# Kernel tuning notes

Measured on AMD Instinct MI355X. Metric: run time of the kernel, lower is better.

The kernel has to match this reference:

```python
import jax, jax.numpy as jnp
import numpy as np

STU, ITEM, CONC, D = 50000, 20000, 2000, 128
E_CC, E_IC, E_SI = 40000, 80000, 1000000


def _gat(tgt_x, src_x, e_src, e_dst, n_tgt, W, att_l, att_r, slope=0.2):
    # single-head GATConv, aggr='add', concat with heads=1 -> [n_tgt, D]
    if W is not None:
        xl = src_x @ W.T  # lin_l applied to source
        xr = tgt_x @ W.T  # lin_l shared for target (in_channels is int)
        # noqa: torch module uses lin_l for both when in_channels is int
    else:
        xl, xr = src_x, tgt_x
    sl = xl @ att_l  # [n_src]
    sr = xr @ att_r  # [n_tgt]
    e = sl[e_src] + sr[e_dst]
    e = jnp.where(e > 0, e, slope * e)  # leaky_relu
    # segment softmax over edges grouped by target node
    m = jax.ops.segment_max(e, e_dst, num_segments=n_tgt)
    m = jnp.where(jnp.isfinite(m), m, 0.0)
    ex = jnp.exp(e - m[e_dst])
    den = jax.ops.segment_sum(ex, e_dst, num_segments=n_tgt) + 1e-16
    alpha = ex / den[e_dst]
    return jax.ops.segment_sum(xl[e_src] * alpha[:, None], e_dst, num_segments=n_tgt)


def setup_inputs():
    key = jax.random.key(0)
    ks = jax.random.split(key, 40)
    s = 1.0 / np.sqrt(D)
    n = lambda k, sh, sc=1.0: jax.random.normal(k, sh, jnp.float32) * sc
    return {
        'stu_x': n(ks[0], (STU, D)),
        'item_x': n(ks[1], (ITEM, D)),
        'conc_x': n(ks[2], (CONC, D)),
        'stu_raw_x': n(ks[3], (STU, D)),
        'W_cc': n(ks[4], (D, D), s), 'al_cc': n(ks[5], (D,), s), 'ar_cc': n(ks[6], (D,), s),
        'W_ic': n(ks[7], (D, D), s), 'al_ic': n(ks[8], (D,), s), 'ar_ic': n(ks[9], (D,), s),
        'al_cce': n(ks[10], (D,), s), 'ar_cce': n(ks[11], (D,), s),
        'al_ice': n(ks[12], (D,), s), 'ar_ice': n(ks[13], (D,), s),
        'W_ci': n(ks[14], (D, D), s), 'al_ci': n(ks[15], (D,), s), 'ar_ci': n(ks[16], (D,), s),
        'W_si': n(ks[17], (D, D), s), 'al_si': n(ks[18], (D,), s), 'ar_si': n(ks[19], (D,), s),
        'w_ci_att': n(ks[20], (2 * D,), s), 'w_si_att': n(ks[21], (2 * D,), s),
        'W_is': n(ks[22], (D, D), s), 'al_is': n(ks[23], (D,), s), 'ar_is': n(ks[24], (D,), s),
        'cc_src': jax.random.randint(ks[25], (E_CC,), 0, CONC),
        'cc_dst': jax.random.randint(ks[26], (E_CC,), 0, CONC),
        'ic_item': jax.random.randint(ks[27], (E_IC,), 0, ITEM),
        'ic_conc': jax.random.randint(ks[28], (E_IC,), 0, CONC),
        'si_stu': jax.random.randint(ks[29], (E_SI,), 0, STU),
        'si_item': jax.random.randint(ks[30], (E_SI,), 0, ITEM),
    }


def reference(stu_x, item_x, conc_x, stu_raw_x,
              W_cc, al_cc, ar_cc, W_ic, al_ic, ar_ic,
              al_cce, ar_cce, al_ice, ar_ice,
              W_ci, al_ci, ar_ci, W_si, al_si, ar_si,
              w_ci_att, w_si_att, W_is, al_is, ar_is,
              cc_src, cc_dst, ic_item, ic_conc, si_stu, si_item):
    # --- concept fusion ---
    c1 = _gat(conc_x, conc_x, cc_src, cc_dst, CONC, W_cc, al_cc, ar_cc)   # inter_conc_conc
    c2 = _gat(conc_x, item_x, ic_item, ic_conc, CONC, W_ic, al_ic, ar_ic) # inter_item_conc
    e1 = _gat(conc_x, c1, cc_src, cc_dst, CONC, None, al_cce, ar_cce)     # exter_conc_conc (no lin)
    e2 = _gat(conc_x, c2, cc_src, cc_dst, CONC, None, al_ice, ar_ice)     # exter_item_conc (no lin)
    conc_fused = conc_x + e1 + e2
    # --- item fusion ---
    i1 = _gat(item_x, conc_x, ic_conc, ic_item, ITEM, W_ci, al_ci, ar_ci) # inter_conc_item
    i2 = _gat(item_x, stu_x, si_stu, si_item, ITEM, W_si, al_si, ar_si)   # inter_stu_item
    # softmax over dim=1 of an [N,1] tensor (as in the torch code): equals 1.0
    att1 = jax.nn.softmax((jnp.concatenate([i1, item_x], axis=1) @ w_ci_att)[:, None], axis=1)
    att2 = jax.nn.softmax((jnp.concatenate([i2, item_x], axis=1) @ w_si_att)[:, None], axis=1)
    item_fused = item_x + att1 * i1 + att2 * i2
    # --- student fusion (uses raw data['stu'].x as target) ---
    s1 = _gat(stu_raw_x, item_x, si_item, si_stu, STU, W_is, al_is, ar_is)
    stu_fused = stu_raw_x + s1
    return (conc_fused, item_fused, stu_fused)
```

## Files before the change

kernel.cpp:

```cpp
#include <hip/hip_runtime.h>

#define CONC_N 2000
#define ITEM_N 20000
#define STU_N  50000
#define NE_CC  40000
#define NE_IC  80000
#define NE_SI  1000000
#define TBUCK  382

typedef unsigned int uint;
typedef unsigned short ushort;
typedef signed char s8;
typedef __attribute__((ext_vector_type(8))) short bf16x8;
typedef __attribute__((ext_vector_type(4))) float f32x4;

__device__ __forceinline__ ushort f2bf(float f) {
  uint u = __float_as_uint(f);
  uint r = (u + 0x7FFFu + ((u >> 16) & 1u)) >> 16;
  return (ushort)r;
}

__device__ __forceinline__ bf16x8 packfrag(float4 lo, float4 hi) {
  union { bf16x8 s; uint u[4]; } p;
  p.u[0] = (uint)f2bf(lo.x) | ((uint)f2bf(lo.y) << 16);
  p.u[1] = (uint)f2bf(lo.z) | ((uint)f2bf(lo.w) << 16);
  p.u[2] = (uint)f2bf(hi.x) | ((uint)f2bf(hi.y) << 16);
  p.u[3] = (uint)f2bf(hi.z) | ((uint)f2bf(hi.w) << 16);
  return p.s;
}


struct CsrG {
  const int* dst; const int* src;
  unsigned* keys; int* srcs; int* offs;
  int E, n, shift, nbuck, tb, sb;
};
struct CsrGs { CsrG g[5]; };


struct ProjDesc { const float* W; const float* a; float* out; };
struct SetupArgs {
  ProjDesc p[10];
  CsrGs G;
  int* pcnt;
  const float* wsrc[5];
  ushort* wdst[5];
};

__global__ __launch_bounds__(256) void setup_k(SetupArgs A) {
  int b = blockIdx.x;
  int tid = threadIdx.x;
  if (b < 10) {
    __shared__ float Wl[128 * 132];
    __shared__ float a_s[128];
    ProjDesc d = A.p[b];
    #pragma unroll
    for (int i = 0; i < 16; ++i) {
      int s = tid + i * 256;
      int row = s >> 5, c4 = s & 31;
      float4 w = *(const float4*)&d.W[s * 4];
      float* dst = &Wl[row * 132 + c4 * 4];
      dst[0] = w.x; dst[1] = w.y; dst[2] = w.z; dst[3] = w.w;
    }
    if (tid < 128) a_s[tid] = d.a[tid];
    __syncthreads();
    if (tid < 128) {
      float acc = 0.f;
      #pragma unroll 4
      for (int j = 0; j < 128; ++j) acc += Wl[j * 132 + tid] * a_s[j];
      d.out[tid] = acc;
    }
    return;
  }
  if (b >= 170) {
    int wi = b - 170;
    const float* Ws = A.wsrc[wi];
    ushort* Wd = A.wdst[wi];
    for (int rec = tid; rec < 2048; rec += 256) {
      int lane = rec & 63;
      int kk = (rec >> 6) & 3;
      int nt = rec >> 8;
      int x = lane & 15, g = lane >> 4;
      const float* src = &Ws[(nt * 16 + x) * 128 + kk * 32 + 4 * g];
      float4 lo = *(const float4*)src;
      float4 hi = *(const float4*)(src + 16);
      bf16x8 pk = packfrag(lo, hi);
      *(bf16x8*)&Wd[rec * 8] = pk;
    }
    return;
  }
  int bsel = b - 10;
  int gi = bsel >> 5, blk = bsel & 31;
  CsrG g = A.G.g[gi];
  __shared__ int lcnt[128];
  if (tid < 128) lcnt[tid] = 0;
  __syncthreads();
  int chunk = (g.E + 31) >> 5;
  int e0 = blk * chunk, e1 = min(g.E, e0 + chunk);
  for (int e = e0 + tid; e < e1; e += 256)
    atomicAdd(&lcnt[g.dst[e] >> g.shift], 1);
  __syncthreads();
  if (tid < 128) A.pcnt[bsel * 128 + tid] = lcnt[tid];
}


__global__ __launch_bounds__(512) void csr_scan(CsrGs G, const int* __restrict__ pcnt,
                                                int* __restrict__ cur, int* __restrict__ bases) {
  __shared__ int lc[TBUCK];
  __shared__ int lb[TBUCK + 5];
  int tid = threadIdx.x, lane = tid & 63, wv = tid >> 6;
  if (tid < TBUCK) {
    int gi = 0;
    #pragma unroll
    for (int k = 1; k < 5; ++k) if (tid >= G.g[k].tb) gi = k;
    int b = tid - G.g[gi].tb;
    int s = 0;
    for (int blk = 0; blk < 32; ++blk) s += pcnt[((gi << 5) + blk) * 128 + b];
    lc[tid] = s;
  }
  __syncthreads();
  if (wv < 5) {
    CsrG g = G.g[wv];
    int carry = 0;
    for (int base = 0; base < g.nbuck; base += 64) {
      int idx = base + lane;
      int v = (idx < g.nbuck) ? lc[g.tb + idx] : 0;
      int incl = v;
      #pragma unroll
      for (int o = 1; o < 64; o <<= 1) {
        int y = __shfl_up(incl, o);
        if (lane >= o) incl += y;
      }
      if (idx < g.nbuck) lb[g.sb + idx] = carry + incl - v;
      carry += __shfl(incl, 63);
    }
    if (lane == 0) lb[g.sb + g.nbuck] = carry;
  }
  __syncthreads();
  if (tid < TBUCK + 5) bases[tid] = lb[tid];
  if (tid < TBUCK) {
    int gi = 0;
    for (int k = 1; k < 5; ++k) if (tid >= G.g[k].tb) gi = k;
    cur[tid] = lb[tid + gi];
  }
  if (tid < 5) G.g[tid].offs[G.g[tid].n] = G.g[tid].E;
}


__device__ void partition_body(const CsrGs& G, int* __restrict__ cur, int gi, int bx,
                               int nbx, unsigned char* smem) {
  CsrG g = G.g[gi];
  unsigned* ck = (unsigned*)smem;
  unsigned char* cb = smem + 16384;
  int* lcnt = (int*)(smem + 20480);
  int* lcur = (int*)(smem + 20992);
  int tid = threadIdx.x;
  unsigned dmask = (1u << g.shift) - 1;
  for (int c0 = bx * 4096; c0 < g.E; c0 += nbx * 4096) {
    if (tid < 128) lcnt[tid] = 0;
    __syncthreads();
    #pragma unroll
    for (int i = 0; i < 16; ++i) {
      int e = c0 + i * 256 + tid;
      if (e < g.E) {
        int d = g.dst[e], s = g.src[e];
        int b = d >> g.shift;
        ck[i * 256 + tid] = ((unsigned)(d & dmask) << 16) | (unsigned)s;
        cb[i * 256 + tid] = (unsigned char)b;
        atomicAdd(&lcnt[b], 1);
      } else cb[i * 256 + tid] = 255;
    }
    __syncthreads();
    if (tid < g.nbuck && lcnt[tid] > 0) lcur[tid] = atomicAdd(&cur[g.tb + tid], lcnt[tid]);
    __syncthreads();
    #pragma unroll
    for (int i = 0; i < 16; ++i) {
      int b = cb[i * 256 + tid];
      if (b != 255) {
        int pos = atomicAdd(&lcur[b], 1);
        g.keys[pos] = ck[i * 256 + tid];
      }
    }
    __syncthreads();
  }
}

__device__ void rdot_body(const float* __restrict__ x, const float* __restrict__ v,
                          float* __restrict__ o, int n, int blk, int nblk) {
  int lane = threadIdx.x & 63;
  int wid = (blk * 256 + threadIdx.x) >> 6;
  int nw = nblk * 4;
  float va = v[lane], vb = v[64 + lane];
  for (int r = wid; r < n; r += nw) {
    float a = x[r * 128 + lane] * va + x[r * 128 + 64 + lane] * vb;
    #pragma unroll
    for (int of = 32; of; of >>= 1) a += __shfl_xor(a, of);
    if (lane == 0) o[r] = a;
  }
}

__global__ __launch_bounds__(256) void mid3_k(CsrGs G, int* cur,
                                              const float* rx, const float* rv,
                                              float* ro, int rnb) {
  __shared__ __align__(16) unsigned char smem[21504];
  int b = blockIdx.x;
  if (b < 600) {
    partition_body(G, cur, b / 120, b % 120, 120, smem);
  } else {
    rdot_body(rx, rv, ro, STU_N, b - 600, rnb);
  }
}


struct GemmDesc { const float* X; s8* Y8; float2* SS; int n, b0;
                  const float* dv[6]; float* dq[6]; int ds[6]; };
struct BigC {
  GemmDesc g[5];
  int gemm_blocks;
};

__device__ void build_lite(const CsrGs& G, const int* __restrict__ bases, int bid,
                           int* lh, int* lex, int* lcu, int* wsum) {
  int gi = 0;
  for (int k = 1; k < 5; ++k) if (bid >= G.g[k].tb) gi = k;
  CsrG g = G.g[gi];
  int b = bid - g.tb;
  int base = bases[g.sb + b];
  int cnt = bases[g.sb + b + 1] - base;

  int tid = threadIdx.x;
  lh[tid] = 0; lh[tid + 256] = 0;
  __syncthreads();
  for (int j = tid; j < cnt; j += 256)
    atomicAdd(&lh[g.keys[base + j] >> 16], 1);
  __syncthreads();
  int a0 = lh[2 * tid], a1 = lh[2 * tid + 1];
  int pair = a0 + a1;
  int lane = tid & 63, wv = tid >> 6;
  int incl = pair;
  #pragma unroll
  for (int o = 1; o < 64; o <<= 1) {
    int y = __shfl_up(incl, o);
    if (lane >= o) incl += y;
  }
  if (lane == 63) wsum[wv] = incl;
  __syncthreads();
  if (tid == 0) {
    int s = 0;
    #pragma unroll
    for (int w = 0; w < 4; ++w) { int t = wsum[w]; wsum[w] = s; s += t; }
  }
  __syncthreads();
  int ep = wsum[wv] + incl - pair;
  lex[2 * tid] = ep;       lex[2 * tid + 1] = ep + a0;
  lcu[2 * tid] = ep;       lcu[2 * tid + 1] = ep + a0;
  __syncthreads();
  int dst0 = b << g.shift;
  int ndst = min(1 << g.shift, g.n - dst0);
  for (int dl = tid; dl < ndst; dl += 256) g.offs[dst0 + dl] = base + lex[dl];
  for (int j = tid; j < cnt; j += 256) {
    unsigned k = g.keys[base + j];
    int dl = k >> 16;
    int pos = atomicAdd(&lcu[dl], 1);
    g.srcs[base + pos] = (int)(k & 0xFFFFu);
  }
}

template <int NV>
__device__ void gemm_bodyT(const GemmDesc& gd, const ushort* __restrict__ Wf, int blk) {
  int tid = threadIdx.x;
  int lane = tid & 63, wv = tid >> 6;
  int x = lane & 15, g = lane >> 4;
  int row = blk * 64 + wv * 16 + x;
  const float* xr = &gd.X[(size_t)(row < gd.n ? row : 0) * 128];
  bf16x8 afrag[4];
  float dacc[NV == 0 ? 1 : NV];
  #pragma unroll
  for (int v = 0; v < NV; ++v) dacc[v] = 0.f;
  #pragma unroll
  for (int kk = 0; kk < 4; ++kk) {
    float4 lo = *(const float4*)&xr[kk * 32 + 4 * g];
    float4 hi = *(const float4*)&xr[kk * 32 + 16 + 4 * g];
    afrag[kk] = packfrag(lo, hi);
    #pragma unroll
    for (int v = 0; v < NV; ++v) {
      const float* vp = gd.dv[v];
      float4 vlo = *(const float4*)&vp[kk * 32 + 4 * g];
      float4 vhi = *(const float4*)&vp[kk * 32 + 16 + 4 * g];
      dacc[v] += lo.x * vlo.x + lo.y * vlo.y + lo.z * vlo.z + lo.w * vlo.w
               + hi.x * vhi.x + hi.y * vhi.y + hi.z * vhi.z + hi.w * vhi.w;
    }
  }
  #pragma unroll
  for (int v = 0; v < NV; ++v) {
    float dsum = dacc[v];
    dsum += __shfl_xor(dsum, 16);
    dsum += __shfl_xor(dsum, 32);
    if (lane < 16 && row < gd.n) gd.dq[v][(size_t)row * gd.ds[v]] = dsum;
  }
  f32x4 acc[8];
  #pragma unroll
  for (int t = 0; t < 8; ++t) acc[t] = (f32x4){0.f, 0.f, 0.f, 0.f};
  #pragma unroll
  for (int nt = 0; nt < 8; ++nt) {
    #pragma unroll
    for (int kk = 0; kk < 4; ++kk) {
      union { uint4 u; bf16x8 s; } bu;
      bu.u = *(const uint4*)&Wf[(size_t)((nt * 4 + kk) * 64 + lane) * 8];
      acc[nt] = __builtin_amdgcn_mfma_f32_16x16x32_bf16(afrag[kk], bu.s, acc[nt], 0, 0, 0);
    }
  }
  int orow = blk * 64 + wv * 16 + 4 * g;
  #pragma unroll
  for (int r = 0; r < 4; ++r) {
    float m8 = 0.f;
    #pragma unroll
    for (int nt = 0; nt < 8; ++nt) m8 = fmaxf(m8, fabsf(acc[nt][r]));
    #pragma unroll
    for (int msk = 1; msk < 16; msk <<= 1) m8 = fmaxf(m8, __shfl_xor(m8, msk));
    int gr = orow + r;
    if (gr < gd.n) {
      float invs = (m8 > 0.f) ? 127.f / m8 : 0.f;
      if (x == 0) gd.SS[gr].y = m8 * (1.f / 127.f);
      #pragma unroll
      for (int nt = 0; nt < 8; ++nt) {
        int q = (int)rintf(acc[nt][r] * invs);
        gd.Y8[(size_t)gr * 128 + nt * 16 + x] = (s8)q;
      }
    }
  }
}

__global__ __launch_bounds__(256, 2) void mid4_k(CsrGs G, const int* bases, BigC C,
                                                 const ushort* W0, const ushort* W1,
                                                 const ushort* W2, const ushort* W3,
                                                 const ushort* W4) {
  __shared__ int lh[512], lex[512], lcu[512], wsum[4];
  int b = blockIdx.x;
  if (b < TBUCK) {
    build_lite(G, bases, b, lh, lex, lcu, wsum);
    return;
  }
  b -= TBUCK;
  if (b < C.g[1].b0)      gemm_bodyT<6>(C.g[0], W0, b - C.g[0].b0);
  else if (b < C.g[2].b0) gemm_bodyT<4>(C.g[1], W1, b - C.g[1].b0);
  else if (b < C.g[3].b0) gemm_bodyT<0>(C.g[2], W2, b - C.g[2].b0);
  else if (b < C.g[4].b0) gemm_bodyT<1>(C.g[3], W3, b - C.g[3].b0);
  else                    gemm_bodyT<0>(C.g[4], W4, b - C.g[4].b0);
}


__device__ __forceinline__ void fma8q(float acc[8], float wj, uint2 u) {
  int lo = (int)u.x, hi = (int)u.y;
  acc[0] += wj * (float)((lo << 24) >> 24);
  acc[1] += wj * (float)((lo << 16) >> 24);
  acc[2] += wj * (float)((lo << 8) >> 24);
  acc[3] += wj * (float)(lo >> 24);
  acc[4] += wj * (float)((hi << 24) >> 24);
  acc[5] += wj * (float)((hi << 16) >> 24);
  acc[6] += wj * (float)((hi << 8) >> 24);
  acc[7] += wj * (float)(hi >> 24);
}

__device__ void gat_core16(const int* __restrict__ offs, const int* __restrict__ srcs,
                           const float2* __restrict__ ssc, const float* __restrict__ sr,
                           const s8* __restrict__ x8,
                           int t4, int n_tgt, int lane, float acc[8]) {
  int q = lane >> 4, il = lane & 15;
  int t = t4 + q;
  bool tv = t < n_tgt;
  int sbeg = tv ? offs[t] : 0;
  int send = tv ? offs[t + 1] : 0;
  float srt = tv ? sr[t] : 0.f;

  float se = 0.f;
  #pragma unroll
  for (int r = 0; r < 8; ++r) acc[r] = 0.f;
  int qb = q << 4;

  for (int i0 = sbeg; i0 < send; i0 += 16) {
    int cnt = min(16, send - i0);
// ... 111 lines not shown
  #pragma unroll
  for (int o = 32; o; o >>= 1) {
    se1 += __shfl_xor(se1, o);
    se2 += __shfl_xor(se2, o);
  }
  float inv1 = 1.f / (se1 + 1e-16f), inv2 = 1.f / (se2 + 1e-16f);
  float ax = 0.f, ay = 0.f;
  for (int i0 = sbeg; i0 < send; i0 += 64) {
    int cnt = min(64, send - i0);
    int s = 0; float w1 = 0.f, w2 = 0.f;
    if (lane < cnt) {
      s = srcs[i0 + lane];
      float e1 = sl1[s] + srt1; e1 = e1 > 0.f ? e1 : 0.2f * e1;
      float e2 = sl2[s] + srt2; e2 = e2 > 0.f ? e2 : 0.2f * e2;
      w1 = __expf(e1 - m1) * inv1;
      w2 = __expf(e2 - m2) * inv2;
    }
    for (int j = 0; j < cnt; ++j) {
      int sj = __shfl(s, j);
      float wj1 = __shfl(w1, j);
      float wj2 = __shfl(w2, j);
      const float2 v1 = *(const float2*)&xl1[sj * 128 + lane * 2];
      const float2 v2 = *(const float2*)&xl2[sj * 128 + lane * 2];
      ax += wj1 * v1.x + wj2 * v2.x;
      ay += wj1 * v1.y + wj2 * v2.y;
    }
  }
  const float2 b = *(const float2*)&base[t * 128 + lane * 2];
  float2 o2; o2.x = ax + b.x; o2.y = ay + b.y;
  *(float2*)&out[t * 128 + lane * 2] = o2;
}


#define NB_I12 1250
#define NB_S1  3125
#define NB_CC  125

struct GatsArgs {
  const int *offs4, *srcs4; const float2* ssc_is; const float* sr_is;
  const s8* x_is; const float* stu_raw_x; float* out_stu;
  const int *offs3, *srcs3; const float2* ssc_si; const float* sr_si; const s8* x_si;
  const int *offs2, *srcs2; const float2* ssc_ci; const float* sr_ci; const s8* x_ci;
  const float* item_x; float* out_item;
  const int *offs0, *srcs0; const float2* ssc_cc; const float* sr_cc; const s8* x_cc;
  const float* al_cce; float *c1, *sl_cce;
  const int *offs1, *srcs1; const float2* ssc_ic; const float* sr_ic; const s8* x_ic;
  const float* al_ice; float *c2, *sl_ice;
};

__global__ void gats_k(GatsArgs A) {
  int b = blockIdx.x;
  int lane = threadIdx.x & 63;
  int wv = threadIdx.x >> 6;
  if (b < NB_I12) {
    int t4 = b * 16 + wv * 4;
    float acc1[8], acc2[8];
    gat_core16(A.offs2, A.srcs2, A.ssc_ci, A.sr_ci, A.x_ci, t4, ITEM_N, lane, acc1);
    gat_core16(A.offs3, A.srcs3, A.ssc_si, A.sr_si, A.x_si, t4, ITEM_N, lane, acc2);
    #pragma unroll
    for (int r = 0; r < 8; ++r) acc1[r] += acc2[r];
    gat_store16(acc1, A.item_x, A.out_item, t4, ITEM_N, lane);
  } else if (b < NB_I12 + NB_S1) {
    int t4 = (b - NB_I12) * 16 + wv * 4;
    float acc[8];
    gat_core16(A.offs4, A.srcs4, A.ssc_is, A.sr_is, A.x_is, t4, STU_N, lane, acc);
    gat_store16(acc, A.stu_raw_x, A.out_stu, t4, STU_N, lane);
  } else {
    int sub = b - NB_I12 - NB_S1;
    int which = sub >= NB_CC;
    int t4 = (sub - which * NB_CC) * 16 + wv * 4;
    if (!which)
      c1c2_body16(A.offs0, A.srcs0, A.ssc_cc, A.sr_cc, A.x_cc, A.al_cce,
                  A.c1, A.sl_cce, t4, CONC_N, lane);
    else
      c1c2_body16(A.offs1, A.srcs1, A.ssc_ic, A.sr_ic, A.x_ic, A.al_ice,
                  A.c2, A.sl_ice, t4, CONC_N, lane);
  }
}


__global__ void fin_k(const int* offs0, const int* srcs0,
                      const float* sl_cce, const float* sr_cce, const float* c1,
                      const float* sl_ice, const float* sr_ice, const float* c2,
                      const float* conc_x, float* out_conc) {
  int t = (blockIdx.x * blockDim.x + threadIdx.x) >> 6;
  if (t >= CONC_N) return;
  gat_dual_core(offs0, srcs0, sl_cce, sr_cce, c1, sl_ice, sr_ice, c2,
                conc_x, out_conc, t, threadIdx.x & 63);
}


extern "C" void kernel_launch(void* const* d_in, const int* in_sizes, int n_in,
                              void* d_out, int out_size, void* d_ws, size_t ws_size,
                              hipStream_t stream) {
  const float* stu_x     = (const float*)d_in[0];
  const float* item_x    = (const float*)d_in[1];
  const float* conc_x    = (const float*)d_in[2];
  const float* stu_raw_x = (const float*)d_in[3];
  const float* W_cc  = (const float*)d_in[4];
  const float* al_cc = (const float*)d_in[5];
  const float* ar_cc = (const float*)d_in[6];
  const float* W_ic  = (const float*)d_in[7];
  const float* al_ic = (const float*)d_in[8];
  const float* ar_ic = (const float*)d_in[9];
  const float* al_cce = (const float*)d_in[10];
  const float* ar_cce = (const float*)d_in[11];
  const float* al_ice = (const float*)d_in[12];
  const float* ar_ice = (const float*)d_in[13];
  const float* W_ci  = (const float*)d_in[14];
  const float* al_ci = (const float*)d_in[15];
  const float* ar_ci = (const float*)d_in[16];
  const float* W_si  = (const float*)d_in[17];
  const float* al_si = (const float*)d_in[18];
  const float* ar_si = (const float*)d_in[19];
  const float* W_is  = (const float*)d_in[22];
  const float* al_is = (const float*)d_in[23];
  const float* ar_is = (const float*)d_in[24];
  const int* cc_src  = (const int*)d_in[25];
  const int* cc_dst  = (const int*)d_in[26];
  const int* ic_item = (const int*)d_in[27];
  const int* ic_conc = (const int*)d_in[28];
// ... 27 lines not shown
  float* sr_ic  = (float*)alloc(CONC_N * 4);
  float* sr_ci  = (float*)alloc(ITEM_N * 4);
  float* sr_si  = (float*)alloc(ITEM_N * 4);
  float* sr_is  = (float*)alloc(STU_N * 4);
  float* sl_cce = (float*)alloc(CONC_N * 4);
  float* sr_cce = (float*)alloc(CONC_N * 4);
  float* sl_ice = (float*)alloc(CONC_N * 4);
  float* sr_ice = (float*)alloc(CONC_N * 4);

  unsigned* keys0 = (unsigned*)alloc((size_t)NE_CC * 4);
  unsigned* keys1 = (unsigned*)alloc((size_t)NE_IC * 4);
  unsigned* keys2 = (unsigned*)alloc((size_t)NE_IC * 4);
  unsigned* keys3 = (unsigned*)alloc((size_t)NE_SI * 4);
  unsigned* keys4 = (unsigned*)alloc((size_t)NE_SI * 4);
  int* srcs0 = (int*)alloc((size_t)NE_CC * 4);
  int* srcs1 = (int*)alloc((size_t)NE_IC * 4);
  int* srcs2 = (int*)alloc((size_t)NE_IC * 4);
  int* srcs3 = (int*)alloc((size_t)NE_SI * 4);
  int* srcs4 = (int*)alloc((size_t)NE_SI * 4);
  int* offs0 = (int*)alloc((CONC_N + 1) * 4);
  int* offs1 = (int*)alloc((CONC_N + 1) * 4);
  int* offs2 = (int*)alloc((ITEM_N + 1) * 4);
  int* offs3 = (int*)alloc((ITEM_N + 1) * 4);
  int* offs4 = (int*)alloc((STU_N + 1) * 4);
  int* pcnt      = (int*)alloc(5 * 32 * 128 * 4);
  int* cur_all   = (int*)alloc(TBUCK * 4);
  int* bases_all = (int*)alloc((TBUCK + 5) * 4);

  float* out = (float*)d_out;
  float* out_conc = out;
  float* out_item = out + (size_t)CONC_N * 128;
  float* out_stu  = out + (size_t)(CONC_N + ITEM_N) * 128;

  CsrGs G;
  G.g[0] = {cc_dst,  cc_src,  keys0, srcs0, offs0, NE_CC, CONC_N, 5, 63,   0,   0};
  G.g[1] = {ic_conc, ic_item, keys1, srcs1, offs1, NE_IC, CONC_N, 5, 63,  63,  64};
  G.g[2] = {ic_item, ic_conc, keys2, srcs2, offs2, NE_IC, ITEM_N, 8, 79, 126, 128};
  G.g[3] = {si_item, si_stu,  keys3, srcs3, offs3, NE_SI, ITEM_N, 8, 79, 205, 208};
  G.g[4] = {si_stu,  si_item, keys4, srcs4, offs4, NE_SI, STU_N,  9, 98, 284, 288};

  SetupArgs SA;
  SA.p[0] = {W_cc, al_cc, vecs + 0 * 128};
  SA.p[1] = {W_cc, ar_cc, vecs + 1 * 128};
  SA.p[2] = {W_ic, al_ic, vecs + 2 * 128};
  SA.p[3] = {W_ic, ar_ic, vecs + 3 * 128};
  SA.p[4] = {W_ci, al_ci, vecs + 4 * 128};
  SA.p[5] = {W_ci, ar_ci, vecs + 5 * 128};
  SA.p[6] = {W_si, al_si, vecs + 6 * 128};
  SA.p[7] = {W_si, ar_si, vecs + 7 * 128};
  SA.p[8] = {W_is, al_is, vecs + 8 * 128};
  SA.p[9] = {W_is, ar_is, vecs + 9 * 128};
  SA.G = G;
  SA.pcnt = pcnt;
  SA.wsrc[0] = W_cc; SA.wsrc[1] = W_ic; SA.wsrc[2] = W_ci;
  SA.wsrc[3] = W_si; SA.wsrc[4] = W_is;
  for (int i = 0; i < 5; ++i) SA.wdst[i] = Wbf[i];
  setup_k<<<175, 256, 0, stream>>>(SA);

  csr_scan<<<1, 512, 0, stream>>>(G, pcnt, cur_all, bases_all);

  mid3_k<<<600 + 1024, 256, 0, stream>>>(G, cur_all, stu_raw_x, vecs + 9 * 128,
                                         sr_is, 1024);

  BigC C;
  C.g[0] = {conc_x, concWcc, ssc_cc, CONC_N, 0,
            {vecs + 0 * 128, vecs + 1 * 128, vecs + 3 * 128, vecs + 4 * 128, ar_cce, ar_ice},
            {(float*)ssc_cc, sr_cc, sr_ic, (float*)ssc_ci, sr_cce, sr_ice},
            {2, 1, 1, 2, 1, 1}};
  C.g[1] = {item_x, itemWic, ssc_ic, ITEM_N, 32,
            {vecs + 2 * 128, vecs + 5 * 128, vecs + 7 * 128, vecs + 8 * 128, nullptr, nullptr},
            {(float*)ssc_ic, sr_ci, sr_si, (float*)ssc_is, nullptr, nullptr},
            {2, 1, 1, 2, 1, 1}};
  C.g[2] = {conc_x, concWci, ssc_ci, CONC_N, 345,
            {nullptr, nullptr, nullptr, nullptr, nullptr, nullptr},
            {nullptr, nullptr, nullptr, nullptr, nullptr, nullptr},
            {1, 1, 1, 1, 1, 1}};
  C.g[3] = {stu_x, stuWsi, ssc_si, STU_N, 377,
            {vecs + 6 * 128, nullptr, nullptr, nullptr, nullptr, nullptr},
            {(float*)ssc_si, nullptr, nullptr, nullptr, nullptr, nullptr},
            {2, 1, 1, 1, 1, 1}};
  C.g[4] = {item_x, itemWis, ssc_is, ITEM_N, 1159,
            {nullptr, nullptr, nullptr, nullptr, nullptr, nullptr},
            {nullptr, nullptr, nullptr, nullptr, nullptr, nullptr},
            {1, 1, 1, 1, 1, 1}};
  C.gemm_blocks = 1472;
  mid4_k<<<TBUCK + 1472, 256, 0, stream>>>(G, bases_all, C,
                                           Wbf[0], Wbf[1], Wbf[2], Wbf[3], Wbf[4]);

  GatsArgs GA;
  GA.offs4 = offs4; GA.srcs4 = srcs4; GA.ssc_is = ssc_is; GA.sr_is = sr_is;
  GA.x_is = itemWis; GA.stu_raw_x = stu_raw_x; GA.out_stu = out_stu;
  GA.offs3 = offs3; GA.srcs3 = srcs3; GA.ssc_si = ssc_si; GA.sr_si = sr_si;
  GA.x_si = stuWsi;
  GA.offs2 = offs2; GA.srcs2 = srcs2; GA.ssc_ci = ssc_ci; GA.sr_ci = sr_ci;
  GA.x_ci = concWci; GA.item_x = item_x; GA.out_item = out_item;
  GA.offs0 = offs0; GA.srcs0 = srcs0; GA.ssc_cc = ssc_cc; GA.sr_cc = sr_cc;
  GA.x_cc = concWcc; GA.al_cce = al_cce; GA.c1 = c1buf; GA.sl_cce = sl_cce;
  GA.offs1 = offs1; GA.srcs1 = srcs1; GA.ssc_ic = ssc_ic; GA.sr_ic = sr_ic;
  GA.x_ic = itemWic; GA.al_ice = al_ice; GA.c2 = c2buf; GA.sl_ice = sl_ice;
  gats_k<<<NB_I12 + NB_S1 + 2 * NB_CC, 256, 0, stream>>>(GA);

  fin_k<<<500, 256, 0, stream>>>(offs0, srcs0, sl_cce, sr_cce, c1buf,
                                 sl_ice, sr_ice, c2buf, conc_x, out_conc);
}
```

Baseline: 173.9 us.

## Fuse all stages into one cooperative persistent kernel with grid syncs

Replaces the six separate kernel launches with a single cooperative kernel that loops over virtual block ids per phase and separates phases with grid.sync(). The build_lite stage is moved out of the GEMM kernel into its own phase after partitioning, and the small projection now reads W directly from global memory instead of staging it in LDS. The goal is to remove launch gaps and per-kernel tail effects. In exchange, the grid size is capped by occupancy, grid-wide barriers add their own cost, the single-block scan phase idles the rest of the grid, and the separate-kernel path is kept as a fallback.

```diff
diff --git a/kernel.cpp b/kernel.cpp
--- a/kernel.cpp
+++ b/kernel.cpp
@@ -1,4 +1,7 @@
 #include <hip/hip_runtime.h>
+#include <hip/hip_cooperative_groups.h>
+
+namespace cg = cooperative_groups;
 
 #define CONC_N 2000
 #define ITEM_N 20000
@@ -8,6 +11,16 @@
 #define NE_SI  1000000
 #define TBUCK  382
 
+#define NB_PART 600
+#define NB_GEMM 1472
+#define NB_RDOT 1024
+#define NB_B    (NB_PART + NB_GEMM + NB_RDOT)
+#define NB_I12  1250
+#define NB_S1   3125
+#define NB_CC   125
+#define NB_D    (NB_I12 + NB_S1 + 2 * NB_CC)
+#define NB_E    500
+
 typedef unsigned int uint;
 typedef unsigned short ushort;
 typedef signed char s8;
@@ -37,62 +50,70 @@
 };
 struct CsrGs { CsrG g[5]; };
 
-
 struct ProjDesc { const float* W; const float* a; float* out; };
-struct SetupArgs {
+
+struct GemmDesc { const float* X; s8* Y8; float2* SS; int n, b0;
+                  const float* dv[6]; float* dq[6]; int ds[6]; };
+struct BigC { GemmDesc g[5]; };
+
+struct GatsArgs {
+  const int *offs4, *srcs4; const float2* ssc_is; const float* sr_is;
+  const s8* x_is; const float* stu_raw_x; float* out_stu;
+  const int *offs3, *srcs3; const float2* ssc_si; const float* sr_si; const s8* x_si;
+  const int *offs2, *srcs2; const float2* ssc_ci; const float* sr_ci; const s8* x_ci;
+  const float* item_x; float* out_item;
+  const int *offs0, *srcs0; const float2* ssc_cc; const float* sr_cc; const s8* x_cc;
+  const float* al_cce; float *c1, *sl_cce;
+  const int *offs1, *srcs1; const float2* ssc_ic; const float* sr_ic; const s8* x_ic;
+  const float* al_ice; float *c2, *sl_ice;
+};
+
+struct MegaArgs {
   ProjDesc p[10];
   CsrGs G;
   int* pcnt;
   const float* wsrc[5];
   ushort* wdst[5];
+  int* cur; int* bases;
+  BigC C;
+  const float* rx; const float* rv; float* ro;
+  GatsArgs GA;
+  const float* sr_cce; const float* sr_ice;
+  const float* conc_x; float* out_conc;
 };
 
-__global__ __launch_bounds__(256) void setup_k(SetupArgs A) {
-  int b = blockIdx.x;
+
+__device__ void proj_body(const ProjDesc& d) {
   int tid = threadIdx.x;
-  if (b < 10) {
-    __shared__ float Wl[128 * 132];
-    __shared__ float a_s[128];
-    ProjDesc d = A.p[b];
-    #pragma unroll
-    for (int i = 0; i < 16; ++i) {
-      int s = tid + i * 256;
-      int row = s >> 5, c4 = s & 31;
-      float4 w = *(const float4*)&d.W[s * 4];
-      float* dst = &Wl[row * 132 + c4 * 4];
-      dst[0] = w.x; dst[1] = w.y; dst[2] = w.z; dst[3] = w.w;
-    }
-    if (tid < 128) a_s[tid] = d.a[tid];
-    __syncthreads();
-    if (tid < 128) {
-      float acc = 0.f;
-      #pragma unroll 4
-      for (int j = 0; j < 128; ++j) acc += Wl[j * 132 + tid] * a_s[j];
-      d.out[tid] = acc;
-    }
-    return;
-  }
-  if (b >= 170) {
-    int wi = b - 170;
-    const float* Ws = A.wsrc[wi];
-    ushort* Wd = A.wdst[wi];
-    for (int rec = tid; rec < 2048; rec += 256) {
-      int lane = rec & 63;
-      int kk = (rec >> 6) & 3;
-      int nt = rec >> 8;
-      int x = lane & 15, g = lane >> 4;
-      const float* src = &Ws[(nt * 16 + x) * 128 + kk * 32 + 4 * g];
-      float4 lo = *(const float4*)src;
-      float4 hi = *(const float4*)(src + 16);
-      bf16x8 pk = packfrag(lo, hi);
-      *(bf16x8*)&Wd[rec * 8] = pk;
-    }
-    return;
-  }
-  int bsel = b - 10;
+  if (tid < 128) {
+    float acc = 0.f;
+    #pragma unroll 4
+    for (int j = 0; j < 128; ++j) acc += d.W[j * 128 + tid] * d.a[j];
+    d.out[tid] = acc;
+  }
+}
+
+__device__ void wconv_body(const float* __restrict__ Ws, ushort* __restrict__ Wd) {
+  int tid = threadIdx.x;
+  for (int rec = tid; rec < 2048; rec += 256) {
+    int lane = rec & 63;
+    int kk = (rec >> 6) & 3;
+    int nt = rec >> 8;
+    int x = lane & 15, g = lane >> 4;
+    const float* src = &Ws[(nt * 16 + x) * 128 + kk * 32 + 4 * g];
+    float4 lo = *(const float4*)src;
+    float4 hi = *(const float4*)(src + 16);
+    bf16x8 pk = packfrag(lo, hi);
+    *(bf16x8*)&Wd[rec * 8] = pk;
+  }
+}
+
+__device__ void hist_body(const CsrGs& G, int* __restrict__ pcnt, int bsel,
+                          unsigned char* smem) {
+  int* lcnt = (int*)smem;
+  int tid = threadIdx.x;
   int gi = bsel >> 5, blk = bsel & 31;
-  CsrG g = A.G.g[gi];
-  __shared__ int lcnt[128];
+  CsrG g = G.g[gi];
   if (tid < 128) lcnt[tid] = 0;
   __syncthreads();
   int chunk = (g.E + 31) >> 5;
@@ -100,52 +121,56 @@
   for (int e = e0 + tid; e < e1; e += 256)
     atomicAdd(&lcnt[g.dst[e] >> g.shift], 1);
   __syncthreads();
-  if (tid < 128) A.pcnt[bsel * 128 + tid] = lcnt[tid];
-}
-
-
-__global__ __launch_bounds__(512) void csr_scan(CsrGs G, const int* __restrict__ pcnt,
-                                                int* __restrict__ cur, int* __restrict__ bases) {
-  __shared__ int lc[TBUCK];
-  __shared__ int lb[TBUCK + 5];
-  int tid = threadIdx.x, lane = tid & 63, wv = tid >> 6;
-  if (tid < TBUCK) {
+  if (tid < 128) pcnt[bsel * 128 + tid] = lcnt[tid];
+  __syncthreads();
+}
+
+__device__ void scan_body(const CsrGs& G, const int* __restrict__ pcnt,
+                          int* __restrict__ cur, int* __restrict__ bases,
+                          unsigned char* smem) {
+  int* lc = (int*)smem;
+  int* lb = (int*)(smem + 2048);
+  int tid = threadIdx.x;
+  for (int i = tid; i < TBUCK; i += 256) {
     int gi = 0;
     #pragma unroll
-    for (int k = 1; k < 5; ++k) if (tid >= G.g[k].tb) gi = k;
-    int b = tid - G.g[gi].tb;
+    for (int k = 1; k < 5; ++k) if (i >= G.g[k].tb) gi = k;
+    int b = i - G.g[gi].tb;
     int s = 0;
     for (int blk = 0; blk < 32; ++blk) s += pcnt[((gi << 5) + blk) * 128 + b];
-    lc[tid] = s;
-  }
-  __syncthreads();
-  if (wv < 5) {
-    CsrG g = G.g[wv];
-    int carry = 0;
-    for (int base = 0; base < g.nbuck; base += 64) {
-      int idx = base + lane;
-      int v = (idx < g.nbuck) ? lc[g.tb + idx] : 0;
-      int incl = v;
-      #pragma unroll
-      for (int o = 1; o < 64; o <<= 1) {
-        int y = __shfl_up(incl, o);
-        if (lane >= o) incl += y;
+    lc[i] = s;
+  }
+  __syncthreads();
+  int lane = tid & 63, wv = tid >> 6;
+  if (wv == 0) {
+    for (int gi = 0; gi < 5; ++gi) {
+      CsrG g = G.g[gi];
+      int carry = 0;
+      for (int base = 0; base < g.nbuck; base += 64) {
+        int idx = base + lane;
+        int v = (idx < g.nbuck) ? lc[g.tb + idx] : 0;
+        int incl = v;
+        #pragma unroll
+        for (int o = 1; o < 64; o <<= 1) {
+          int y = __shfl_up(incl, o);
+          if (lane >= o) incl += y;
+        }
+        if (idx < g.nbuck) lb[g.sb + idx] = carry + incl - v;
+        carry += __shfl(incl, 63);
       }
-      if (idx < g.nbuck) lb[g.sb + idx] = carry + incl - v;
-      carry += __shfl(incl, 63);
-    }
-    if (lane == 0) lb[g.sb + g.nbuck] = carry;
-  }
-  __syncthreads();
-  if (tid < TBUCK + 5) bases[tid] = lb[tid];
-  if (tid < TBUCK) {
+      if (lane == 0) lb[g.sb + g.nbuck] = carry;
+    }
+  }
+  __syncthreads();
+  for (int i = tid; i < TBUCK + 5; i += 256) bases[i] = lb[i];
+  for (int i = tid; i < TBUCK; i += 256) {
     int gi = 0;
-    for (int k = 1; k < 5; ++k) if (tid >= G.g[k].tb) gi = k;
-    cur[tid] = lb[tid + gi];
+    for (int k = 1; k < 5; ++k) if (i >= G.g[k].tb) gi = k;
+    cur[i] = lb[i + gi];
   }
   if (tid < 5) G.g[tid].offs[G.g[tid].n] = G.g[tid].E;
-}
-
+  __syncthreads();
+}
 
 __device__ void partition_body(const CsrGs& G, int* __restrict__ cur, int gi, int bx,
                                int nbx, unsigned char* smem) {
@@ -199,73 +224,6 @@
   }
 }
 
-__global__ __launch_bounds__(256) void mid3_k(CsrGs G, int* cur,
-                                              const float* rx, const float* rv,
-                                              float* ro, int rnb) {
-  __shared__ __align__(16) unsigned char smem[21504];
-  int b = blockIdx.x;
-  if (b < 600) {
-    partition_body(G, cur, b / 120, b % 120, 120, smem);
-  } else {
-    rdot_body(rx, rv, ro, STU_N, b - 600, rnb);
-  }
-}
-
-
-struct GemmDesc { const float* X; s8* Y8; float2* SS; int n, b0;
-                  const float* dv[6]; float* dq[6]; int ds[6]; };
-struct BigC {
-  GemmDesc g[5];
-  int gemm_blocks;
-};
-
-__device__ void build_lite(const CsrGs& G, const int* __restrict__ bases, int bid,
-                           int* lh, int* lex, int* lcu, int* wsum) {
-  int gi = 0;
-  for (int k = 1; k < 5; ++k) if (bid >= G.g[k].tb) gi = k;
-  CsrG g = G.g[gi];
-  int b = bid - g.tb;
-  int base = bases[g.sb + b];
-  int cnt = bases[g.sb + b + 1] - base;
-
-  int tid = threadIdx.x;
-  lh[tid] = 0; lh[tid + 256] = 0;
-  __syncthreads();
-  for (int j = tid; j < cnt; j += 256)
-    atomicAdd(&lh[g.keys[base + j] >> 16], 1);
-  __syncthreads();
-  int a0 = lh[2 * tid], a1 = lh[2 * tid + 1];
-  int pair = a0 + a1;
-  int lane = tid & 63, wv = tid >> 6;
-  int incl = pair;
-  #pragma unroll
-  for (int o = 1; o < 64; o <<= 1) {
-    int y = __shfl_up(incl, o);
-    if (lane >= o) incl += y;
-  }
-  if (lane == 63) wsum[wv] = incl;
-  __syncthreads();
-  if (tid == 0) {
-    int s = 0;
-    #pragma unroll
-    for (int w = 0; w < 4; ++w) { int t = wsum[w]; wsum[w] = s; s += t; }
-  }
-  __syncthreads();
-  int ep = wsum[wv] + incl - pair;
-  lex[2 * tid] = ep;       lex[2 * tid + 1] = ep + a0;
-  lcu[2 * tid] = ep;       lcu[2 * tid + 1] = ep + a0;
-  __syncthreads();
-  int dst0 = b << g.shift;
-  int ndst = min(1 << g.shift, g.n - dst0);
-  for (int dl = tid; dl < ndst; dl += 256) g.offs[dst0 + dl] = base + lex[dl];
-  for (int j = tid; j < cnt; j += 256) {
-    unsigned k = g.keys[base + j];
-    int dl = k >> 16;
-    int pos = atomicAdd(&lcu[dl], 1);
-    g.srcs[base + pos] = (int)(k & 0xFFFFu);
-  }
-}
-
 template <int NV>
 __device__ void gemm_bodyT(const GemmDesc& gd, const ushort* __restrict__ Wf, int blk) {
   int tid = threadIdx.x;
@@ -331,22 +289,56 @@
   }
 }
 
-__global__ __launch_bounds__(256, 2) void mid4_k(CsrGs G, const int* bases, BigC C,
-                                                 const ushort* W0, const ushort* W1,
-                                                 const ushort* W2, const ushort* W3,
-                                                 const ushort* W4) {
-  __shared__ int lh[512], lex[512], lcu[512], wsum[4];
-  int b = blockIdx.x;
-  if (b < TBUCK) {
-    build_lite(G, bases, b, lh, lex, lcu, wsum);
-    return;
-  }
-  b -= TBUCK;
-  if (b < C.g[1].b0)      gemm_bodyT<6>(C.g[0], W0, b - C.g[0].b0);
-  else if (b < C.g[2].b0) gemm_bodyT<4>(C.g[1], W1, b - C.g[1].b0);
-  else if (b < C.g[3].b0) gemm_bodyT<0>(C.g[2], W2, b - C.g[2].b0);
-  else if (b < C.g[4].b0) gemm_bodyT<1>(C.g[3], W3, b - C.g[3].b0);
-  else                    gemm_bodyT<0>(C.g[4], W4, b - C.g[4].b0);
+__device__ void build_lite(const CsrGs& G, const int* __restrict__ bases, int bid,
+                           unsigned char* smem) {
+  int* lh = (int*)smem;
+  int* lex = (int*)(smem + 2048);
+  int* lcu = (int*)(smem + 4096);
+  int* wsum = (int*)(smem + 6144);
+  int gi = 0;
+  for (int k = 1; k < 5; ++k) if (bid >= G.g[k].tb) gi = k;
+  CsrG g = G.g[gi];
+  int b = bid - g.tb;
+  int base = bases[g.sb + b];
+  int cnt = bases[g.sb + b + 1] - base;
+
+  int tid = threadIdx.x;
+  lh[tid] = 0; lh[tid + 256] = 0;
+  __syncthreads();
+  for (int j = tid; j < cnt; j += 256)
+    atomicAdd(&lh[g.keys[base + j] >> 16], 1);
+  __syncthreads();
+  int a0 = lh[2 * tid], a1 = lh[2 * tid + 1];
+  int pair = a0 + a1;
+  int lane = tid & 63, wv = tid >> 6;
+  int incl = pair;
+  #pragma unroll
+  for (int o = 1; o < 64; o <<= 1) {
+    int y = __shfl_up(incl, o);
+    if (lane >= o) incl += y;
+  }
+  if (lane == 63) wsum[wv] = incl;
+  __syncthreads();
+  if (tid == 0) {
+    int s = 0;
+    #pragma unroll
+    for (int w = 0; w < 4; ++w) { int t = wsum[w]; wsum[w] = s; s += t; }
+  }
+  __syncthreads();
+  int ep = wsum[wv] + incl - pair;
+  lex[2 * tid] = ep;       lex[2 * tid + 1] = ep + a0;
+  lcu[2 * tid] = ep;       lcu[2 * tid + 1] = ep + a0;
+  __syncthreads();
+  int dst0 = b << g.shift;
+  int ndst = min(1 << g.shift, g.n - dst0);
+  for (int dl = tid; dl < ndst; dl += 256) g.offs[dst0 + dl] = base + lex[dl];
+  for (int j = tid; j < cnt; j += 256) {
+    unsigned k = g.keys[base + j];
+    int dl = k >> 16;
+    int pos = atomicAdd(&lcu[dl], 1);
+    g.srcs[base + pos] = (int)(k & 0xFFFFu);
+  }
+  __syncthreads();
 }
 
 
@@ -524,61 +516,106 @@
 }
 
 
-#define NB_I12 1250
-#define NB_S1  3125
-#define NB_CC  125
-
-struct GatsArgs {
-  const int *offs4, *srcs4; const float2* ssc_is; const float* sr_is;
-  const s8* x_is; const float* stu_raw_x; float* out_stu;
-  const int *offs3, *srcs3; const float2* ssc_si; const float* sr_si; const s8* x_si;
-  const int *offs2, *srcs2; const float2* ssc_ci; const float* sr_ci; const s8* x_ci;
-  const float* item_x; float* out_item;
-  const int *offs0, *srcs0; const float2* ssc_cc; const float* sr_cc; const s8* x_cc;
-  const float* al_cce; float *c1, *sl_cce;
-  const int *offs1, *srcs1; const float2* ssc_ic; const float* sr_ic; const s8* x_ic;
-  const float* al_ice; float *c2, *sl_ice;
-};
-
-__global__ void gats_k(GatsArgs A) {
-  int b = blockIdx.x;
+__device__ void phaseA(const MegaArgs& A, int vb, unsigned char* smem) {
+  if (vb < 10) proj_body(A.p[vb]);
+  else if (vb >= 170) wconv_body(A.wsrc[vb - 170], A.wdst[vb - 170]);
+  else hist_body(A.G, A.pcnt, vb - 10, smem);
+}
+
+__device__ void phaseB(const MegaArgs& A, int vb, unsigned char* smem) {
+  if (vb < NB_PART) {
+    partition_body(A.G, A.cur, vb / 120, vb % 120, 120, smem);
+  } else if (vb < NB_PART + NB_GEMM) {
+    int b = vb - NB_PART;
+    const BigC& C = A.C;
+    if (b < C.g[1].b0)      gemm_bodyT<6>(C.g[0], A.wdst[0], b - C.g[0].b0);
+    else if (b < C.g[2].b0) gemm_bodyT<4>(C.g[1], A.wdst[1], b - C.g[1].b0);
+    else if (b < C.g[3].b0) gemm_bodyT<0>(C.g[2], A.wdst[2], b - C.g[2].b0);
+    else if (b < C.g[4].b0) gemm_bodyT<1>(C.g[3], A.wdst[3], b - C.g[3].b0);
+    else                    gemm_bodyT<0>(C.g[4], A.wdst[4], b - C.g[4].b0);
+  } else {
+    rdot_body(A.rx, A.rv, A.ro, STU_N, vb - NB_PART - NB_GEMM, NB_RDOT);
+  }
+}
+
+__device__ void phaseD(const MegaArgs& A, int vb) {
+  const GatsArgs& GA = A.GA;
   int lane = threadIdx.x & 63;
   int wv = threadIdx.x >> 6;
-  if (b < NB_I12) {
-    int t4 = b * 16 + wv * 4;
+  if (vb < NB_I12) {
+    int t4 = vb * 16 + wv * 4;
     float acc1[8], acc2[8];
-    gat_core16(A.offs2, A.srcs2, A.ssc_ci, A.sr_ci, A.x_ci, t4, ITEM_N, lane, acc1);
-    gat_core16(A.offs3, A.srcs3, A.ssc_si, A.sr_si, A.x_si, t4, ITEM_N, lane, acc2);
+    gat_core16(GA.offs2, GA.srcs2, GA.ssc_ci, GA.sr_ci, GA.x_ci, t4, ITEM_N, lane, acc1);
+    gat_core16(GA.offs3, GA.srcs3, GA.ssc_si, GA.sr_si, GA.x_si, t4, ITEM_N, lane, acc2);
     #pragma unroll
     for (int r = 0; r < 8; ++r) acc1[r] += acc2[r];
-    gat_store16(acc1, A.item_x, A.out_item, t4, ITEM_N, lane);
-  } else if (b < NB_I12 + NB_S1) {
-    int t4 = (b - NB_I12) * 16 + wv * 4;
+    gat_store16(acc1, GA.item_x, GA.out_item, t4, ITEM_N, lane);
+  } else if (vb < NB_I12 + NB_S1) {
+    int t4 = (vb - NB_I12) * 16 + wv * 4;
     float acc[8];
-    gat_core16(A.offs4, A.srcs4, A.ssc_is, A.sr_is, A.x_is, t4, STU_N, lane, acc);
-    gat_store16(acc, A.stu_raw_x, A.out_stu, t4, STU_N, lane);
+    gat_core16(GA.offs4, GA.srcs4, GA.ssc_is, GA.sr_is, GA.x_is, t4, STU_N, lane, acc);
+    gat_store16(acc, GA.stu_raw_x, GA.out_stu, t4, STU_N, lane);
   } else {
-    int sub = b - NB_I12 - NB_S1;
+    int sub = vb - NB_I12 - NB_S1;
     int which = sub >= NB_CC;
     int t4 = (sub - which * NB_CC) * 16 + wv * 4;
     if (!which)
-      c1c2_body16(A.offs0, A.srcs0, A.ssc_cc, A.sr_cc, A.x_cc, A.al_cce,
-                  A.c1, A.sl_cce, t4, CONC_N, lane);
+      c1c2_body16(GA.offs0, GA.srcs0, GA.ssc_cc, GA.sr_cc, GA.x_cc, GA.al_cce,
+                  GA.c1, GA.sl_cce, t4, CONC_N, lane);
     else
-      c1c2_body16(A.offs1, A.srcs1, A.ssc_ic, A.sr_ic, A.x_ic, A.al_ice,
-                  A.c2, A.sl_ice, t4, CONC_N, lane);
-  }
-}
-
-
-__global__ void fin_k(const int* offs0, const int* srcs0,
-                      const float* sl_cce, const float* sr_cce, const float* c1,
-                      const float* sl_ice, const float* sr_ice, const float* c2,
-                      const float* conc_x, float* out_conc) {
-  int t = (blockIdx.x * blockDim.x + threadIdx.x) >> 6;
-  if (t >= CONC_N) return;
-  gat_dual_core(offs0, srcs0, sl_cce, sr_cce, c1, sl_ice, sr_ice, c2,
-                conc_x, out_conc, t, threadIdx.x & 63);
+      c1c2_body16(GA.offs1, GA.srcs1, GA.ssc_ic, GA.sr_ic, GA.x_ic, GA.al_ice,
+                  GA.c2, GA.sl_ice, t4, CONC_N, lane);
+  }
+}
+
+__device__ void phaseE(const MegaArgs& A, int vb) {
+  int t = (vb * 256 + (int)threadIdx.x) >> 6;
+  if (t < CONC_N)
+    gat_dual_core(A.GA.offs0, A.GA.srcs0, A.GA.sl_cce, A.sr_cce, A.GA.c1,
+                  A.GA.sl_ice, A.sr_ice, A.GA.c2, A.conc_x, A.out_conc,
+                  t, threadIdx.x & 63);
+}
+
+
+__global__ __launch_bounds__(256, 4) void mega_k(MegaArgs A) {
+  __shared__ __align__(16) unsigned char smem[21504];
+  cg::grid_group grid = cg::this_grid();
+  int nb = gridDim.x;
+  for (int vb = blockIdx.x; vb < 175; vb += nb) phaseA(A, vb, smem);
+  grid.sync();
+  if (blockIdx.x == 0) scan_body(A.G, A.pcnt, A.cur, A.bases, smem);
+  grid.sync();
+  for (int vb = blockIdx.x; vb < NB_B; vb += nb) phaseB(A, vb, smem);
+  grid.sync();
+  for (int vb = blockIdx.x; vb < TBUCK; vb += nb) build_lite(A.G, A.bases, vb, smem);
+  grid.sync();
+  for (int vb = blockIdx.x; vb < NB_D; vb += nb) phaseD(A, vb);
+  grid.sync();
+  for (int vb = blockIdx.x; vb < NB_E; vb += nb) phaseE(A, vb);
+}
+
+
+__global__ __launch_bounds__(256) void f_A(MegaArgs A) {
+  __shared__ __align__(16) unsigned char smem[21504];
+  phaseA(A, blockIdx.x, smem);
+}
+__global__ __launch_bounds__(256) void f_scan(MegaArgs A) {
+  __shared__ __align__(16) unsigned char smem[8192];
+  scan_body(A.G, A.pcnt, A.cur, A.bases, smem);
+}
+__global__ __launch_bounds__(256, 2) void f_B(MegaArgs A) {
+  __shared__ __align__(16) unsigned char smem[21504];
+  phaseB(A, blockIdx.x, smem);
+}
+__global__ __launch_bounds__(256) void f_C(MegaArgs A) {
+  __shared__ __align__(16) unsigned char smem[8192];
+  build_lite(A.G, A.bases, blockIdx.x, smem);
+}
+__global__ __launch_bounds__(256) void f_D(MegaArgs A) {
+  phaseD(A, blockIdx.x);
+}
+__global__ __launch_bounds__(256) void f_E(MegaArgs A) {
+  phaseE(A, blockIdx.x);
 }
 
 
@@ -672,74 +709,75 @@
   float* out_item = out + (size_t)CONC_N * 128;
   float* out_stu  = out + (size_t)(CONC_N + ITEM_N) * 128;
 
-  CsrGs G;
-  G.g[0] = {cc_dst,  cc_src,  keys0, srcs0, offs0, NE_CC, CONC_N, 5, 63,   0,   0};
-  G.g[1] = {ic_conc, ic_item, keys1, srcs1, offs1, NE_IC, CONC_N, 5, 63,  63,  64};
-  G.g[2] = {ic_item, ic_conc, keys2, srcs2, offs2, NE_IC, ITEM_N, 8, 79, 126, 128};
-  G.g[3] = {si_item, si_stu,  keys3, srcs3, offs3, NE_SI, ITEM_N, 8, 79, 205, 208};
-  G.g[4] = {si_stu,  si_item, keys4, srcs4, offs4, NE_SI, STU_N,  9, 98, 284, 288};
-
-  SetupArgs SA;
-  SA.p[0] = {W_cc, al_cc, vecs + 0 * 128};
-  SA.p[1] = {W_cc, ar_cc, vecs + 1 * 128};
-  SA.p[2] = {W_ic, al_ic, vecs + 2 * 128};
-  SA.p[3] = {W_ic, ar_ic, vecs + 3 * 128};
-  SA.p[4] = {W_ci, al_ci, vecs + 4 * 128};
-  SA.p[5] = {W_ci, ar_ci, vecs + 5 * 128};
-  SA.p[6] = {W_si, al_si, vecs + 6 * 128};
-  SA.p[7] = {W_si, ar_si, vecs + 7 * 128};
-  SA.p[8] = {W_is, al_is, vecs + 8 * 128};
-  SA.p[9] = {W_is, ar_is, vecs + 9 * 128};
-  SA.G = G;
-  SA.pcnt = pcnt;
-  SA.wsrc[0] = W_cc; SA.wsrc[1] = W_ic; SA.wsrc[2] = W_ci;
-  SA.wsrc[3] = W_si; SA.wsrc[4] = W_is;
-  for (int i = 0; i < 5; ++i) SA.wdst[i] = Wbf[i];
-  setup_k<<<175, 256, 0, stream>>>(SA);
-
-  csr_scan<<<1, 512, 0, stream>>>(G, pcnt, cur_all, bases_all);
-
-  mid3_k<<<600 + 1024, 256, 0, stream>>>(G, cur_all, stu_raw_x, vecs + 9 * 128,
-                                         sr_is, 1024);
-
-  BigC C;
-  C.g[0] = {conc_x, concWcc, ssc_cc, CONC_N, 0,
-            {vecs + 0 * 128, vecs + 1 * 128, vecs + 3 * 128, vecs + 4 * 128, ar_cce, ar_ice},
-            {(float*)ssc_cc, sr_cc, sr_ic, (float*)ssc_ci, sr_cce, sr_ice},
-            {2, 1, 1, 2, 1, 1}};
-  C.g[1] = {item_x, itemWic, ssc_ic, ITEM_N, 32,
-            {vecs + 2 * 128, vecs + 5 * 128, vecs + 7 * 128, vecs + 8 * 128, nullptr, nullptr},
-            {(float*)ssc_ic, sr_ci, sr_si, (float*)ssc_is, nullptr, nullptr},
-            {2, 1, 1, 2, 1, 1}};
-  C.g[2] = {conc_x, concWci, ssc_ci, CONC_N, 345,
-            {nullptr, nullptr, nullptr, nullptr, nullptr, nullptr},
-            {nullptr, nullptr, nullptr, nullptr, nullptr, nullptr},
-            {1, 1, 1, 1, 1, 1}};
-  C.g[3] = {stu_x, stuWsi, ssc_si, STU_N, 377,
-            {vecs + 6 * 128, nullptr, nullptr, nullptr, nullptr, nullptr},
-            {(float*)ssc_si, nullptr, nullptr, nullptr, nullptr, nullptr},
-            {2, 1, 1, 1, 1, 1}};
-  C.g[4] = {item_x, itemWis, ssc_is, ITEM_N, 1159,
-            {nullptr, nullptr, nullptr, nullptr, nullptr, nullptr},
-            {nullptr, nullptr, nullptr, nullptr, nullptr, nullptr},
-            {1, 1, 1, 1, 1, 1}};
-  C.gemm_blocks = 1472;
-  mid4_k<<<TBUCK + 1472, 256, 0, stream>>>(G, bases_all, C,
-                                           Wbf[0], Wbf[1], Wbf[2], Wbf[3], Wbf[4]);
-
-  GatsArgs GA;
-  GA.offs4 = offs4; GA.srcs4 = srcs4; GA.ssc_is = ssc_is; GA.sr_is = sr_is;
-  GA.x_is = itemWis; GA.stu_raw_x = stu_raw_x; GA.out_stu = out_stu;
-  GA.offs3 = offs3; GA.srcs3 = srcs3; GA.ssc_si = ssc_si; GA.sr_si = sr_si;
-  GA.x_si = stuWsi;
-  GA.offs2 = offs2; GA.srcs2 = srcs2; GA.ssc_ci = ssc_ci; GA.sr_ci = sr_ci;
-  GA.x_ci = concWci; GA.item_x = item_x; GA.out_item = out_item;
-  GA.offs0 = offs0; GA.srcs0 = srcs0; GA.ssc_cc = ssc_cc; GA.sr_cc = sr_cc;
-  GA.x_cc = concWcc; GA.al_cce = al_cce; GA.c1 = c1buf; GA.sl_cce = sl_cce;
-  GA.offs1 = offs1; GA.srcs1 = srcs1; GA.ssc_ic = ssc_ic; GA.sr_ic = sr_ic;
-  GA.x_ic = itemWic; GA.al_ice = al_ice; GA.c2 = c2buf; GA.sl_ice = sl_ice;
-  gats_k<<<NB_I12 + NB_S1 + 2 * NB_CC, 256, 0, stream>>>(GA);
-
-  fin_k<<<500, 256, 0, stream>>>(offs0, srcs0, sl_cce, sr_cce, c1buf,
-                                 sl_ice, sr_ice, c2buf, conc_x, out_conc);
-}
+  MegaArgs A;
+  A.p[0] = {W_cc, al_cc, vecs + 0 * 128};
+  A.p[1] = {W_cc, ar_cc, vecs + 1 * 128};
+  A.p[2] = {W_ic, al_ic, vecs + 2 * 128};
+  A.p[3] = {W_ic, ar_ic, vecs + 3 * 128};
+  A.p[4] = {W_ci, al_ci, vecs + 4 * 128};
+  A.p[5] = {W_ci, ar_ci, vecs + 5 * 128};
+  A.p[6] = {W_si, al_si, vecs + 6 * 128};
+  A.p[7] = {W_si, ar_si, vecs + 7 * 128};
+  A.p[8] = {W_is, al_is, vecs + 8 * 128};
+  A.p[9] = {W_is, ar_is, vecs + 9 * 128};
+  A.G.g[0] = {cc_dst,  cc_src,  keys0, srcs0, offs0, NE_CC, CONC_N, 5, 63,   0,   0};
+  A.G.g[1] = {ic_conc, ic_item, keys1, srcs1, offs1, NE_IC, CONC_N, 5, 63,  63,  64};
+  A.G.g[2] = {ic_item, ic_conc, keys2, srcs2, offs2, NE_IC, ITEM_N, 8, 79, 126, 128};
+  A.G.g[3] = {si_item, si_stu,  keys3, srcs3, offs3, NE_SI, ITEM_N, 8, 79, 205, 208};
+  A.G.g[4] = {si_stu,  si_item, keys4, srcs4, offs4, NE_SI, STU_N,  9, 98, 284, 288};
+  A.pcnt = pcnt;
+  A.wsrc[0] = W_cc; A.wsrc[1] = W_ic; A.wsrc[2] = W_ci;
+  A.wsrc[3] = W_si; A.wsrc[4] = W_is;
+  for (int i = 0; i < 5; ++i) A.wdst[i] = Wbf[i];
+  A.cur = cur_all; A.bases = bases_all;
+  A.C.g[0] = {conc_x, concWcc, ssc_cc, CONC_N, 0,
+              {vecs + 0 * 128, vecs + 1 * 128, vecs + 3 * 128, vecs + 4 * 128, ar_cce, ar_ice},
+              {(float*)ssc_cc, sr_cc, sr_ic, (float*)ssc_ci, sr_cce, sr_ice},
+              {2, 1, 1, 2, 1, 1}};
+  A.C.g[1] = {item_x, itemWic, ssc_ic, ITEM_N, 32,
+              {vecs + 2 * 128, vecs + 5 * 128, vecs + 7 * 128, vecs + 8 * 128, nullptr, nullptr},
+              {(float*)ssc_ic, sr_ci, sr_si, (float*)ssc_is, nullptr, nullptr},
+              {2, 1, 1, 2, 1, 1}};
+  A.C.g[2] = {conc_x, concWci, ssc_ci, CONC_N, 345,
+              {nullptr, nullptr, nullptr, nullptr, nullptr, nullptr},
+              {nullptr, nullptr, nullptr, nullptr, nullptr, nullptr},
+              {1, 1, 1, 1, 1, 1}};
+  A.C.g[3] = {stu_x, stuWsi, ssc_si, STU_N, 377,
+              {vecs + 6 * 128, nullptr, nullptr, nullptr, nullptr, nullptr},
+              {(float*)ssc_si, nullptr, nullptr, nullptr, nullptr, nullptr},
+              {2, 1, 1, 1, 1, 1}};
+  A.C.g[4] = {item_x, itemWis, ssc_is, ITEM_N, 1159,
+              {nullptr, nullptr, nullptr, nullptr, nullptr, nullptr},
+              {nullptr, nullptr, nullptr, nullptr, nullptr, nullptr},
+              {1, 1, 1, 1, 1, 1}};
+  A.rx = stu_raw_x; A.rv = vecs + 9 * 128; A.ro = sr_is;
+  A.GA.offs4 = offs4; A.GA.srcs4 = srcs4; A.GA.ssc_is = ssc_is; A.GA.sr_is = sr_is;
+  A.GA.x_is = itemWis; A.GA.stu_raw_x = stu_raw_x; A.GA.out_stu = out_stu;
+  A.GA.offs3 = offs3; A.GA.srcs3 = srcs3; A.GA.ssc_si = ssc_si; A.GA.sr_si = sr_si;
+  A.GA.x_si = stuWsi;
+  A.GA.offs2 = offs2; A.GA.srcs2 = srcs2; A.GA.ssc_ci = ssc_ci; A.GA.sr_ci = sr_ci;
+  A.GA.x_ci = concWci; A.GA.item_x = item_x; A.GA.out_item = out_item;
+  A.GA.offs0 = offs0; A.GA.srcs0 = srcs0; A.GA.ssc_cc = ssc_cc; A.GA.sr_cc = sr_cc;
+  A.GA.x_cc = concWcc; A.GA.al_cce = al_cce; A.GA.c1 = c1buf; A.GA.sl_cce = sl_cce;
+  A.GA.offs1 = offs1; A.GA.srcs1 = srcs1; A.GA.ssc_ic = ssc_ic; A.GA.sr_ic = sr_ic;
+  A.GA.x_ic = itemWic; A.GA.al_ice = al_ice; A.GA.c2 = c2buf; A.GA.sl_ice = sl_ice;
+  A.sr_cce = sr_cce; A.sr_ice = sr_ice;
+  A.conc_x = conc_x; A.out_conc = out_conc;
+
+  int maxb = 0;
+  hipError_t oe = hipOccupancyMaxActiveBlocksPerMultiprocessor(&maxb, mega_k, 256, 0);
+  if (oe != hipSuccess || maxb < 1) maxb = 4;
+  int grid = maxb * 256;
+  if (grid > NB_D) grid = NB_D;
+  void* kargs[] = { (void*)&A };
+  hipError_t le = hipLaunchCooperativeKernel((void*)mega_k, dim3(grid), dim3(256),
+                                             kargs, 0, stream);
+  if (le != hipSuccess) {
+    f_A<<<175, 256, 0, stream>>>(A);
+    f_scan<<<1, 256, 0, stream>>>(A);
+    f_B<<<NB_B, 256, 0, stream>>>(A);
+    f_C<<<TBUCK, 256, 0, stream>>>(A);
+    f_D<<<NB_D, 256, 0, stream>>>(A);
+    f_E<<<NB_E, 256, 0, stream>>>(A);
+  }
+}
```

Result: slower. 596.5 us (+243.0%).
